# Optimization experiments

Hardware: AMD Instinct MI355X
Metric: run time of the kernel (lower is better)

The kernel has to match this reference:

```python
import jax, jax.numpy as jnp
import numpy as np


def setup_inputs() -> dict:
    key = jax.random.key(0)
    # frames: stack of 4 feature maps, each [B, C, H, W]
    frames = jax.random.normal(key, (4, 8, 64, 160, 160), dtype=jnp.float32)
    return {"frames": frames}


def reference(frames) -> jnp.ndarray:
    # frames: [4, B, C, H, W]
    B, C = frames.shape[1], frames.shape[2]
    # V = cat(x1..x4, dim=1) -> [B, 4C, H, W]
    V = jnp.concatenate([frames[i] for i in range(4)], axis=1)
    outs = []
    for i in range(4):
        # Qi = cat([xi]*4, dim=1) -> [B, 4C, H, W]
        Qi = jnp.tile(frames[i], (1, 4, 1, 1))
        # softmax over the 4C channel axis, then gate V
        s = jax.nn.softmax(Qi * V, axis=1) * V  # [B, 4C, H, W]
        # chunk into 4 blocks of C channels and sum -> [B, C, H, W]
        outs.append(s.reshape(B, 4, C, *s.shape[2:]).sum(axis=1))
    return jnp.concatenate(outs, axis=1)  # [B, 4C, H, W]
```

## Files before the change

### kernel.cpp

```cpp
#include <hip/hip_runtime.h>


#define HW 25600
#define NP 16
#define ROW 260
#define TILES_PER_B 1600

__device__ __forceinline__ float wave_allsum(float x) {
  int v;
  v = __builtin_amdgcn_update_dpp(0, __float_as_int(x), 0xB1, 0xf, 0xf, true);
  x += __int_as_float(v);
  v = __builtin_amdgcn_update_dpp(0, __float_as_int(x), 0x4E, 0xf, 0xf, true);
  x += __int_as_float(v);
  v = __builtin_amdgcn_update_dpp(0, __float_as_int(x), 0x141, 0xf, 0xf, true);
  x += __int_as_float(v);
  v = __builtin_amdgcn_update_dpp(0, __float_as_int(x), 0x140, 0xf, 0xf, true);
  x += __int_as_float(v);
  v = __builtin_amdgcn_update_dpp(0, __float_as_int(x), 0x142, 0xa, 0xf, false);
  x += __int_as_float(v);
  v = __builtin_amdgcn_update_dpp(0, __float_as_int(x), 0x143, 0xc, 0xf, false);
  x += __int_as_float(v);
  return __int_as_float(__builtin_amdgcn_readlane(__float_as_int(x), 63));
}

__global__ __launch_bounds__(256, 6) void fused_frame_softmax(
    const float* __restrict__ in, float* __restrict__ out) {
  __shared__ float Xs[NP * ROW];

  const int b  = blockIdx.x / TILES_PER_B;
  const int p0 = (blockIdx.x % TILES_PER_B) * NP;
  const int t  = threadIdx.x;

  #pragma unroll
  for (int it = 0; it < 4; ++it) {
    const int q  = it * 256 + t;
    const int ch = q >> 2;
    const int pq = (q & 3) << 2;
    const int j  = ch >> 6;
    const int c  = ch & 63;
    const float4 v = *reinterpret_cast<const float4*>(
        in + ((j * 8 + b) * 64 + c) * HW + p0 + pq);
    Xs[(pq + 0) * ROW + ch] = v.x;
    Xs[(pq + 1) * ROW + ch] = v.y;
    Xs[(pq + 2) * ROW + ch] = v.z;
    Xs[(pq + 3) * ROW + ch] = v.w;
  }
  __syncthreads();

  const int lane  = t & 63;
  const int wbase = (t >> 6) * 4;
  #pragma unroll 1
  for (int pp = 0; pp < 4; ++pp) {
    float* row = Xs + (wbase + pp) * ROW;
    const float x0 = row[lane];
    const float x1 = row[lane + 64];
    const float x2 = row[lane + 128];
    const float x3 = row[lane + 192];

    const float L = 1.4426950408889634f;
    const float y0 = x0 * L, y1 = x1 * L, y2 = x2 * L, y3 = x3 * L;
    const float E00 = __builtin_amdgcn_exp2f(y0 * x0);
    const float E01 = __builtin_amdgcn_exp2f(y0 * x1);
    const float E02 = __builtin_amdgcn_exp2f(y0 * x2);
    const float E03 = __builtin_amdgcn_exp2f(y0 * x3);
    const float E11 = __builtin_amdgcn_exp2f(y1 * x1);
    const float E12 = __builtin_amdgcn_exp2f(y1 * x2);
    const float E13 = __builtin_amdgcn_exp2f(y1 * x3);
    const float E22 = __builtin_amdgcn_exp2f(y2 * x2);
    const float E23 = __builtin_amdgcn_exp2f(y2 * x3);
    const float E33 = __builtin_amdgcn_exp2f(y3 * x3);

    const float z0 = wave_allsum(E00 + E01 + E02 + E03);
    const float z1 = wave_allsum(E01 + E11 + E12 + E13);
    const float z2 = wave_allsum(E02 + E12 + E22 + E23);
    const float z3 = wave_allsum(E03 + E13 + E23 + E33);

    const float r0 = __builtin_amdgcn_rcpf(z0);
    const float r1 = __builtin_amdgcn_rcpf(z1);
    const float r2 = __builtin_amdgcn_rcpf(z2);
    const float r3 = __builtin_amdgcn_rcpf(z3);

    row[lane]       = (E00 * x0 + E01 * x1 + E02 * x2 + E03 * x3) * r0;
    row[lane + 64]  = (E01 * x0 + E11 * x1 + E12 * x2 + E13 * x3) * r1;
    row[lane + 128] = (E02 * x0 + E12 * x1 + E22 * x2 + E23 * x3) * r2;
    row[lane + 192] = (E03 * x0 + E13 * x1 + E23 * x2 + E33 * x3) * r3;
  }
  __syncthreads();

  #pragma unroll
  for (int it = 0; it < 4; ++it) {
    const int q  = it * 256 + t;
    const int ch = q >> 2;
    const int pq = (q & 3) << 2;
    float4 v;
    v.x = Xs[(pq + 0) * ROW + ch];
    v.y = Xs[(pq + 1) * ROW + ch];
    v.z = Xs[(pq + 2) * ROW + ch];
    v.w = Xs[(pq + 3) * ROW + ch];
    *reinterpret_cast<float4*>(out + (b * 256 + ch) * HW + p0 + pq) = v;
  }
}

extern "C" void kernel_launch(void* const* d_in, const int* in_sizes, int n_in,
                              void* d_out, int out_size, void* d_ws, size_t ws_size,
                              hipStream_t stream) {
  const float* in = (const float*)d_in[0];
  float* out      = (float*)d_out;
  fused_frame_softmax<<<dim3(8 * TILES_PER_B), dim3(256), 0, stream>>>(in, out);
}
```

Measured before the change: 396.0 us.

## Make kernel persistent with register prefetch of next tile during compute

Switches from one block per 16-pixel tile to a persistent grid of 1024 blocks, each looping over 32-pixel tiles. While computing the current tile, the next tile's global loads are issued into registers, then written into shared memory after the output store. The aim is to hide global load latency and cut block launch overhead. In exchange, register pressure rises from the 8 prefetched float4s, the occupancy hint drops from 6 to 4 blocks per SM, and tile size changes, so the kernel may end up with fewer waves in flight on a memory-bound problem.

```diff
diff --git a/kernel.cpp b/kernel.cpp
--- a/kernel.cpp
+++ b/kernel.cpp
@@ -2,9 +2,11 @@
 
 
 #define HW 25600
-#define NP 16
-#define ROW 260
-#define TILES_PER_B 1600
+#define NP 32
+#define ROW 258
+#define TILES_PER_B 800
+#define TILES 6400
+#define NBLK 1024
 
 __device__ __forceinline__ float wave_allsum(float x) {
   int v;
@@ -23,81 +25,112 @@
   return __int_as_float(__builtin_amdgcn_readlane(__float_as_int(x), 63));
 }
 
-__global__ __launch_bounds__(256, 6) void fused_frame_softmax(
+__global__ __launch_bounds__(256, 4) void fused_frame_softmax(
     const float* __restrict__ in, float* __restrict__ out) {
   __shared__ float Xs[NP * ROW];
 
-  const int b  = blockIdx.x / TILES_PER_B;
-  const int p0 = (blockIdx.x % TILES_PER_B) * NP;
-  const int t  = threadIdx.x;
+  const int t    = threadIdx.x;
+  const int lane = t & 63;
+  const int wb   = (t >> 6) * 8;
+  const int chb  = t >> 3;
+  const int pq   = (t & 7) << 2;
 
-  #pragma unroll
-  for (int it = 0; it < 4; ++it) {
-    const int q  = it * 256 + t;
-    const int ch = q >> 2;
-    const int pq = (q & 3) << 2;
-    const int j  = ch >> 6;
-    const int c  = ch & 63;
-    const float4 v = *reinterpret_cast<const float4*>(
-        in + ((j * 8 + b) * 64 + c) * HW + p0 + pq);
-    Xs[(pq + 0) * ROW + ch] = v.x;
-    Xs[(pq + 1) * ROW + ch] = v.y;
-    Xs[(pq + 2) * ROW + ch] = v.z;
-    Xs[(pq + 3) * ROW + ch] = v.w;
+  {
+    const int tile = blockIdx.x;
+    const int b  = tile / TILES_PER_B;
+    const int p0 = (tile % TILES_PER_B) * NP;
+    const float* src = in + b * (64 * HW) + p0;
+    #pragma unroll
+    for (int it = 0; it < 8; ++it) {
+      const int ch = it * 32 + chb;
+      const int j = ch >> 6, c = ch & 63;
+      const float4 v = *reinterpret_cast<const float4*>(
+          src + j * (8 * 64 * HW) + c * HW + pq);
+      Xs[(pq + 0) * ROW + ch] = v.x;
+      Xs[(pq + 1) * ROW + ch] = v.y;
+      Xs[(pq + 2) * ROW + ch] = v.z;
+      Xs[(pq + 3) * ROW + ch] = v.w;
+    }
   }
   __syncthreads();
 
-  const int lane  = t & 63;
-  const int wbase = (t >> 6) * 4;
-  #pragma unroll 1
-  for (int pp = 0; pp < 4; ++pp) {
-    float* row = Xs + (wbase + pp) * ROW;
-    const float x0 = row[lane];
-    const float x1 = row[lane + 64];
-    const float x2 = row[lane + 128];
-    const float x3 = row[lane + 192];
+  for (int tile = blockIdx.x; tile < TILES; tile += NBLK) {
+    const int  next     = tile + NBLK;
+    const bool has_next = next < TILES;
+    float4 pre[8];
+    if (has_next) {
+      const int b  = next / TILES_PER_B;
+      const int p0 = (next % TILES_PER_B) * NP;
+      const float* src = in + b * (64 * HW) + p0;
+      #pragma unroll
+      for (int it = 0; it < 8; ++it) {
+        const int ch = it * 32 + chb;
+        const int j = ch >> 6, c = ch & 63;
+        pre[it] = *reinterpret_cast<const float4*>(
+            src + j * (8 * 64 * HW) + c * HW + pq);
+      }
+    }
 
-    const float L = 1.4426950408889634f;
-    const float y0 = x0 * L, y1 = x1 * L, y2 = x2 * L, y3 = x3 * L;
-    const float E00 = __builtin_amdgcn_exp2f(y0 * x0);
-    const float E01 = __builtin_amdgcn_exp2f(y0 * x1);
-    const float E02 = __builtin_amdgcn_exp2f(y0 * x2);
-    const float E03 = __builtin_amdgcn_exp2f(y0 * x3);
-    const float E11 = __builtin_amdgcn_exp2f(y1 * x1);
-    const float E12 = __builtin_amdgcn_exp2f(y1 * x2);
-    const float E13 = __builtin_amdgcn_exp2f(y1 * x3);
-    const float E22 = __builtin_amdgcn_exp2f(y2 * x2);
-    const float E23 = __builtin_amdgcn_exp2f(y2 * x3);
-    const float E33 = __builtin_amdgcn_exp2f(y3 * x3);
+    #pragma unroll 1
+    for (int pp = 0; pp < 8; ++pp) {
+      float* row = Xs + (wb + pp) * ROW;
+      const float x0 = row[lane];
+      const float x1 = row[lane + 64];
+      const float x2 = row[lane + 128];
+      const float x3 = row[lane + 192];
 
-    const float z0 = wave_allsum(E00 + E01 + E02 + E03);
-    const float z1 = wave_allsum(E01 + E11 + E12 + E13);
-    const float z2 = wave_allsum(E02 + E12 + E22 + E23);
-    const float z3 = wave_allsum(E03 + E13 + E23 + E33);
+      const float L = 1.4426950408889634f;
+      const float y0 = x0 * L, y1 = x1 * L, y2 = x2 * L, y3 = x3 * L;
+      const float E00 = __builtin_amdgcn_exp2f(y0 * x0);
+      const float E01 = __builtin_amdgcn_exp2f(y0 * x1);
+      const float E02 = __builtin_amdgcn_exp2f(y0 * x2);
+      const float E03 = __builtin_amdgcn_exp2f(y0 * x3);
+      const float E11 = __builtin_amdgcn_exp2f(y1 * x1);
+      const float E12 = __builtin_amdgcn_exp2f(y1 * x2);
+      const float E13 = __builtin_amdgcn_exp2f(y1 * x3);
+      const float E22 = __builtin_amdgcn_exp2f(y2 * x2);
+      const float E23 = __builtin_amdgcn_exp2f(y2 * x3);
+      const float E33 = __builtin_amdgcn_exp2f(y3 * x3);
 
-    const float r0 = __builtin_amdgcn_rcpf(z0);
-    const float r1 = __builtin_amdgcn_rcpf(z1);
-    const float r2 = __builtin_amdgcn_rcpf(z2);
-    const float r3 = __builtin_amdgcn_rcpf(z3);
+      const float z0 = wave_allsum(E00 + E01 + E02 + E03);
+      const float z1 = wave_allsum(E01 + E11 + E12 + E13);
+      const float z2 = wave_allsum(E02 + E12 + E22 + E23);
+      const float z3 = wave_allsum(E03 + E13 + E23 + E33);
 
-    row[lane]       = (E00 * x0 + E01 * x1 + E02 * x2 + E03 * x3) * r0;
-    row[lane + 64]  = (E01 * x0 + E11 * x1 + E12 * x2 + E13 * x3) * r1;
-    row[lane + 128] = (E02 * x0 + E12 * x1 + E22 * x2 + E23 * x3) * r2;
-    row[lane + 192] = (E03 * x0 + E13 * x1 + E23 * x2 + E33 * x3) * r3;
-  }
-  __syncthreads();
+      const float r0 = __builtin_amdgcn_rcpf(z0);
+      const float r1 = __builtin_amdgcn_rcpf(z1);
+      const float r2 = __builtin_amdgcn_rcpf(z2);
+      const float r3 = __builtin_amdgcn_rcpf(z3);
 
-  #pragma unroll
-  for (int it = 0; it < 4; ++it) {
-    const int q  = it * 256 + t;
-    const int ch = q >> 2;
-    const int pq = (q & 3) << 2;
-    float4 v;
-    v.x = Xs[(pq + 0) * ROW + ch];
-    v.y = Xs[(pq + 1) * ROW + ch];
-    v.z = Xs[(pq + 2) * ROW + ch];
-    v.w = Xs[(pq + 3) * ROW + ch];
-    *reinterpret_cast<float4*>(out + (b * 256 + ch) * HW + p0 + pq) = v;
+      row[lane]       = (E00 * x0 + E01 * x1 + E02 * x2 + E03 * x3) * r0;
+      row[lane + 64]  = (E01 * x0 + E11 * x1 + E12 * x2 + E13 * x3) * r1;
+      row[lane + 128] = (E02 * x0 + E12 * x1 + E22 * x2 + E23 * x3) * r2;
+      row[lane + 192] = (E03 * x0 + E13 * x1 + E23 * x2 + E33 * x3) * r3;
+    }
+    __syncthreads();
+
+    {
+      const int b  = tile / TILES_PER_B;
+      const int p0 = (tile % TILES_PER_B) * NP;
+      float* dst = out + b * (256 * HW) + p0;
+      #pragma unroll
+      for (int it = 0; it < 8; ++it) {
+        const int ch = it * 32 + chb;
+        float4 v;
+        v.x = Xs[(pq + 0) * ROW + ch];
+        v.y = Xs[(pq + 1) * ROW + ch];
+        v.z = Xs[(pq + 2) * ROW + ch];
+        v.w = Xs[(pq + 3) * ROW + ch];
+        *reinterpret_cast<float4*>(dst + ch * HW + pq) = v;
+        if (has_next) {
+          Xs[(pq + 0) * ROW + ch] = pre[it].x;
+          Xs[(pq + 1) * ROW + ch] = pre[it].y;
+          Xs[(pq + 2) * ROW + ch] = pre[it].z;
+          Xs[(pq + 3) * ROW + ch] = pre[it].w;
+        }
+      }
+    }
+    __syncthreads();
   }
 }
 
@@ -106,5 +139,5 @@
                               hipStream_t stream) {
   const float* in = (const float*)d_in[0];
   float* out      = (float*)d_out;
-  fused_frame_softmax<<<dim3(8 * TILES_PER_B), dim3(256), 0, stream>>>(in, out);
+  fused_frame_softmax<<<dim3(NBLK), dim3(256), 0, stream>>>(in, out);
 }
```

Measured after the change: 367.8 us. 1.08x faster.

## Assign one pixel per thread, loop channels, write unnormalized then rescale

Applied to the files above, without the earlier changes.

Replaces the shared-memory tile transpose and cross-lane DPP reductions with a per-thread pixel mapping. Each thread streams all 64 channels of the four frames with a one-step register prefetch and accumulates the softmax denominators locally. It writes the unnormalized outputs, then re-reads and scales them by the reciprocal in a second pass. This removes LDS traffic, syncs and wave reductions, but adds a full extra read-modify-write of the output (about 1.5x the DRAM traffic) and launches only 800 blocks, which limits memory-level parallelism.

```diff
diff --git a/kernel.cpp b/kernel.cpp
--- a/kernel.cpp
+++ b/kernel.cpp
@@ -2,62 +2,36 @@
 
 
 #define HW 25600
-#define NP 16
-#define ROW 260
-#define TILES_PER_B 1600
+#define WPB 400
+#define BLOCK 256
+#define NBLK 800
 
-__device__ __forceinline__ float wave_allsum(float x) {
-  int v;
-  v = __builtin_amdgcn_update_dpp(0, __float_as_int(x), 0xB1, 0xf, 0xf, true);
-  x += __int_as_float(v);
-  v = __builtin_amdgcn_update_dpp(0, __float_as_int(x), 0x4E, 0xf, 0xf, true);
-  x += __int_as_float(v);
-  v = __builtin_amdgcn_update_dpp(0, __float_as_int(x), 0x141, 0xf, 0xf, true);
-  x += __int_as_float(v);
-  v = __builtin_amdgcn_update_dpp(0, __float_as_int(x), 0x140, 0xf, 0xf, true);
-  x += __int_as_float(v);
-  v = __builtin_amdgcn_update_dpp(0, __float_as_int(x), 0x142, 0xa, 0xf, false);
-  x += __int_as_float(v);
-  v = __builtin_amdgcn_update_dpp(0, __float_as_int(x), 0x143, 0xc, 0xf, false);
-  x += __int_as_float(v);
-  return __int_as_float(__builtin_amdgcn_readlane(__float_as_int(x), 63));
-}
+__global__ __launch_bounds__(256) void fused_frame_softmax(
+    const float* __restrict__ in, float* __restrict__ out) {
+  const int wave = blockIdx.x * (BLOCK / 64) + (threadIdx.x >> 6);
+  const int lane = threadIdx.x & 63;
+  const int b    = wave / WPB;
+  const int p    = (wave % WPB) * 64 + lane;
 
-__global__ __launch_bounds__(256, 6) void fused_frame_softmax(
-    const float* __restrict__ in, float* __restrict__ out) {
-  __shared__ float Xs[NP * ROW];
+  const float* in0 = in + (0 * 8 + b) * 64 * HW + p;
+  const float* in1 = in + (1 * 8 + b) * 64 * HW + p;
+  const float* in2 = in + (2 * 8 + b) * 64 * HW + p;
+  const float* in3 = in + (3 * 8 + b) * 64 * HW + p;
+  float* o = out + b * 256 * HW + p;
 
-  const int b  = blockIdx.x / TILES_PER_B;
-  const int p0 = (blockIdx.x % TILES_PER_B) * NP;
-  const int t  = threadIdx.x;
+  const float L = 1.4426950408889634f;
+  float z0 = 0.f, z1 = 0.f, z2 = 0.f, z3 = 0.f;
 
-  #pragma unroll
-  for (int it = 0; it < 4; ++it) {
-    const int q  = it * 256 + t;
-    const int ch = q >> 2;
-    const int pq = (q & 3) << 2;
-    const int j  = ch >> 6;
-    const int c  = ch & 63;
-    const float4 v = *reinterpret_cast<const float4*>(
-        in + ((j * 8 + b) * 64 + c) * HW + p0 + pq);
-    Xs[(pq + 0) * ROW + ch] = v.x;
-    Xs[(pq + 1) * ROW + ch] = v.y;
-    Xs[(pq + 2) * ROW + ch] = v.z;
-    Xs[(pq + 3) * ROW + ch] = v.w;
-  }
-  __syncthreads();
+  float x0 = in0[0], x1 = in1[0], x2 = in2[0], x3 = in3[0];
 
-  const int lane  = t & 63;
-  const int wbase = (t >> 6) * 4;
-  #pragma unroll 1
-  for (int pp = 0; pp < 4; ++pp) {
-    float* row = Xs + (wbase + pp) * ROW;
-    const float x0 = row[lane];
-    const float x1 = row[lane + 64];
-    const float x2 = row[lane + 128];
-    const float x3 = row[lane + 192];
+  #pragma unroll 4
+  for (int c = 0; c < 64; ++c) {
+    const int cn = (c < 63) ? c + 1 : 63;
+    const float n0 = in0[cn * HW];
+    const float n1 = in1[cn * HW];
+    const float n2 = in2[cn * HW];
+    const float n3 = in3[cn * HW];
 
-    const float L = 1.4426950408889634f;
     const float y0 = x0 * L, y1 = x1 * L, y2 = x2 * L, y3 = x3 * L;
     const float E00 = __builtin_amdgcn_exp2f(y0 * x0);
     const float E01 = __builtin_amdgcn_exp2f(y0 * x1);
@@ -70,34 +44,32 @@
     const float E23 = __builtin_amdgcn_exp2f(y2 * x3);
     const float E33 = __builtin_amdgcn_exp2f(y3 * x3);
 
-    const float z0 = wave_allsum(E00 + E01 + E02 + E03);
-    const float z1 = wave_allsum(E01 + E11 + E12 + E13);
-    const float z2 = wave_allsum(E02 + E12 + E22 + E23);
-    const float z3 = wave_allsum(E03 + E13 + E23 + E33);
+    z0 += (E00 + E01) + (E02 + E03);
+    z1 += (E01 + E11) + (E12 + E13);
+    z2 += (E02 + E12) + (E22 + E23);
+    z3 += (E03 + E13) + (E23 + E33);
 
-    const float r0 = __builtin_amdgcn_rcpf(z0);
-    const float r1 = __builtin_amdgcn_rcpf(z1);
-    const float r2 = __builtin_amdgcn_rcpf(z2);
-    const float r3 = __builtin_amdgcn_rcpf(z3);
+    o[(0 * 64 + c) * HW] = E00 * x0 + E01 * x1 + E02 * x2 + E03 * x3;
+    o[(1 * 64 + c) * HW] = E01 * x0 + E11 * x1 + E12 * x2 + E13 * x3;
+    o[(2 * 64 + c) * HW] = E02 * x0 + E12 * x1 + E22 * x2 + E23 * x3;
+    o[(3 * 64 + c) * HW] = E03 * x0 + E13 * x1 + E23 * x2 + E33 * x3;
 
-    row[lane]       = (E00 * x0 + E01 * x1 + E02 * x2 + E03 * x3) * r0;
-    row[lane + 64]  = (E01 * x0 + E11 * x1 + E12 * x2 + E13 * x3) * r1;
-    row[lane + 128] = (E02 * x0 + E12 * x1 + E22 * x2 + E23 * x3) * r2;
-    row[lane + 192] = (E03 * x0 + E13 * x1 + E23 * x2 + E33 * x3) * r3;
+    x0 = n0; x1 = n1; x2 = n2; x3 = n3;
   }
-  __syncthreads();
 
-  #pragma unroll
-  for (int it = 0; it < 4; ++it) {
-    const int q  = it * 256 + t;
-    const int ch = q >> 2;
-    const int pq = (q & 3) << 2;
-    float4 v;
-    v.x = Xs[(pq + 0) * ROW + ch];
-    v.y = Xs[(pq + 1) * ROW + ch];
-    v.z = Xs[(pq + 2) * ROW + ch];
-    v.w = Xs[(pq + 3) * ROW + ch];
-    *reinterpret_cast<float4*>(out + (b * 256 + ch) * HW + p0 + pq) = v;
+  asm volatile("s_waitcnt vmcnt(0)" ::: "memory");
+
+  const float r0 = __builtin_amdgcn_rcpf(z0);
+  const float r1 = __builtin_amdgcn_rcpf(z1);
+  const float r2 = __builtin_amdgcn_rcpf(z2);
+  const float r3 = __builtin_amdgcn_rcpf(z3);
+
+  #pragma unroll 4
+  for (int c = 0; c < 64; ++c) {
+    o[(0 * 64 + c) * HW] *= r0;
+    o[(1 * 64 + c) * HW] *= r1;
+    o[(2 * 64 + c) * HW] *= r2;
+    o[(3 * 64 + c) * HW] *= r3;
   }
 }
 
@@ -106,5 +78,5 @@
                               hipStream_t stream) {
   const float* in = (const float*)d_in[0];
   float* out      = (float*)d_out;
-  fused_frame_softmax<<<dim3(8 * TILES_PER_B), dim3(256), 0, stream>>>(in, out);
+  fused_frame_softmax<<<dim3(NBLK), dim3(BLOCK), 0, stream>>>(in, out);
 }
```

Measured after the change: 448.7 us. 13.3% more time.
